# Kernel tuning notes

Measured on AMD Instinct MI355X. Metric: run time of the kernel, lower is better.

The kernel has to match this reference:

```python
import jax, jax.numpy as jnp
import numpy as np

DIM = 1024
H = 16
DH = DIM // H
LN_EPS = 1e-5


def _linear_params(key, din, dout):
    kw, kb = jax.random.split(key)
    bound = 1.0 / np.sqrt(din)
    W = jax.random.uniform(kw, (din, dout), jnp.float32, -bound, bound)
    b = jax.random.uniform(kb, (dout,), jnp.float32, -bound, bound)
    return W, b


def setup_inputs() -> dict:
    key = jax.random.key(0)
    ks = jax.random.split(key, 10)
    inp = {
        "Q": jax.random.normal(ks[0], (8, 512, DIM), jnp.float32),
        "K1": jax.random.normal(ks[1], (8, 1024, DIM), jnp.float32),
        "K2": jax.random.normal(ks[2], (8, 1024, DIM), jnp.float32),
    }
    for name, k in zip(["q", "k1", "k2", "v1", "v2", "o"], ks[3:9]):
        W, b = _linear_params(k, DIM, DIM)
        inp["W" + name] = W
        inp["b" + name] = b
    inp["g0"] = jnp.ones((DIM,), jnp.float32)
    inp["beta0"] = jnp.zeros((DIM,), jnp.float32)
    inp["g1"] = jnp.ones((DIM,), jnp.float32)
    inp["beta1"] = jnp.zeros((DIM,), jnp.float32)
    return inp


def _layernorm(x, g, b):
    m = jnp.mean(x, axis=-1, keepdims=True)
    v = jnp.mean(jnp.square(x - m), axis=-1, keepdims=True)
    return (x - m) * jax.lax.rsqrt(v + LN_EPS) * g + b


def _split_heads(x):
    # torch.cat(x.split(dh, 2), dim=0): [B,N,D] -> [H*B, N, dh], head-major on axis 0
    B, N, _ = x.shape
    return x.reshape(B, N, H, DH).transpose(2, 0, 1, 3).reshape(H * B, N, DH)


def _merge_heads(x, B):
    # inverse: torch.cat(out.split(B, 0), 2)
    _, N, _ = x.shape
    return x.reshape(H, B, N, DH).transpose(1, 2, 0, 3).reshape(B, N, DIM)


def reference(Q, K1, K2, Wq, bq, Wk1, bk1, Wk2, bk2, Wv1, bv1, Wv2, bv2, Wo, bo, g0, beta0, g1, beta1):
    B = Q.shape[0]
    Qp = Q @ Wq + bq
    # NOTE: faithful to source — V is computed from the ALREADY key-projected K_dict
    K1p = K1 @ Wk1 + bk1
    K2p = K2 @ Wk2 + bk2
    V1p = K1p @ Wv1 + bv1
    V2p = K2p @ Wv2 + bv2
    Q_ = _split_heads(Qp)                                   # [H*B, Nq, dh]
    K_ = jnp.concatenate([_split_heads(K1p), _split_heads(K2p)], axis=1)  # [H*B, Nk, dh]
    V_ = jnp.concatenate([_split_heads(V1p), _split_heads(V2p)], axis=1)
    scores = jnp.einsum("bqd,bkd->bqk", Q_, K_) / np.sqrt(DIM).astype(np.float32)
    # NOTE: faithful to source — softmax over the QUERY axis (dim=1)
    A = jax.nn.softmax(scores, axis=1)
    out = Q_ + jnp.einsum("bqk,bkd->bqd", A, V_)
    out = _merge_heads(out, B)                              # [B, Nq, DIM]
    out = _layernorm(out, g0, beta0)
    out = out + jax.nn.relu(out @ Wo + bo)
    out = _layernorm(out, g1, beta1)
    return out
```

## Files before the change

### kernel.cpp

```cpp
#include <hip/hip_runtime.h>
#include <math.h>

typedef __attribute__((ext_vector_type(8))) _Float16 half8v;
typedef __attribute__((ext_vector_type(4))) _Float16 half4v;
typedef __attribute__((ext_vector_type(4))) float f32x4;

__device__ __forceinline__ void gload16(const void* g, void* l) {
  __builtin_amdgcn_global_load_lds(
      (const __attribute__((address_space(1))) void*)g,
      (__attribute__((address_space(3))) void*)l, 16, 0, 0);
}

struct WP { const float* src; _Float16* dst; };
struct WPArgs { WP w[6]; };

__global__ __launch_bounds__(256)
void wprep_kernel(WPArgs args) {
  __shared__ float tile[32][33];
  const WP wp = args.w[blockIdx.z];
  const int t  = threadIdx.x;
  const int r  = t >> 3;
  const int c  = (t & 7) * 4;
  const int n0 = blockIdx.x * 32;
  const int k0 = blockIdx.y * 32;
  float4 v = *(const float4*)(wp.src + (size_t)(k0 + r) * 1024 + n0 + c);
  tile[r][c] = v.x; tile[r][c + 1] = v.y; tile[r][c + 2] = v.z; tile[r][c + 3] = v.w;
  __syncthreads();
  half4v h;
  #pragma unroll
  for (int i = 0; i < 4; ++i) h[i] = (_Float16)tile[c + i][r];
  *(half4v*)(wp.dst + (size_t)(n0 + r) * 1024 + k0 + c) = h;
}

__global__ __launch_bounds__(256)
void aconv_kernel(const float* __restrict__ in, _Float16* __restrict__ out, int n4) {
  int i = blockIdx.x * 256 + threadIdx.x;
  if (i >= n4) return;
  float4 v = ((const float4*)in)[i];
  half4v o;
  o[0] = (_Float16)v.x; o[1] = (_Float16)v.y; o[2] = (_Float16)v.z; o[3] = (_Float16)v.w;
  ((half4v*)out)[i] = o;
}

template<int MODE>
__global__ __launch_bounds__(256)
void gemm_fp16(const _Float16* __restrict__ A, const _Float16* __restrict__ B,
               const float* __restrict__ bias, const _Float16* __restrict__ X,
               _Float16* __restrict__ C, float* __restrict__ Cf,
               _Float16* __restrict__ Vt) {
  __shared__ _Float16 sA[8192];
  __shared__ _Float16 sB[8192];
  const int t    = threadIdx.x;
  const int bn   = blockIdx.x * 128;
  const int bm   = blockIdx.y * 128;
  const int lane = t & 63;
  const int w    = t >> 6;
  const int wr   = (w >> 1) * 64;
  const int wc   = (w & 1) * 64;
  const int lm   = lane & 15;
  const int lq   = lane >> 4;

  f32x4 acc[4][4];
  #pragma unroll
  for (int i = 0; i < 4; ++i)
    #pragma unroll
    for (int j = 0; j < 4; ++j) { f32x4 z = {0.f, 0.f, 0.f, 0.f}; acc[i][j] = z; }

  for (int k0 = 0; k0 < 1024; k0 += 64) {
    __syncthreads();
    #pragma unroll
    for (int i = 0; i < 4; ++i) {
      const int T    = w * 4 + i;
      const int kq   = T >> 1;
      const int row  = (T & 1) * 64 + lane;
      gload16(A + (size_t)(bm + row) * 1024 + k0 + kq * 8, &sA[(T * 64 + lane) * 8]);
      gload16(B + (size_t)(bn + row) * 1024 + k0 + kq * 8, &sB[(T * 64 + lane) * 8]);
    }
    __syncthreads();

    #pragma unroll
    for (int kk = 0; kk < 2; ++kk) {
      half8v af[4], bf[4];
      #pragma unroll
      for (int mi = 0; mi < 4; ++mi)
        af[mi] = *(const half8v*)&sA[((kk * 4 + lq) * 128 + wr + mi * 16 + lm) * 8];
      #pragma unroll
      for (int ni = 0; ni < 4; ++ni)
        bf[ni] = *(const half8v*)&sB[((kk * 4 + lq) * 128 + wc + ni * 16 + lm) * 8];
      #pragma unroll
      for (int mi = 0; mi < 4; ++mi)
        #pragma unroll
        for (int ni = 0; ni < 4; ++ni)
          acc[mi][ni] = __builtin_amdgcn_mfma_f32_16x16x32_f16(af[mi], bf[ni], acc[mi][ni], 0, 0, 0);
    }
  }

  float bv[4];
  #pragma unroll
  for (int ni = 0; ni < 4; ++ni) bv[ni] = bias[bn + wc + ni * 16 + lm];

  #pragma unroll
  for (int mi = 0; mi < 4; ++mi)
    #pragma unroll
    for (int ni = 0; ni < 4; ++ni) {
      const int col = bn + wc + ni * 16 + lm;
      if (MODE == 2) {
        const int row0 = bm + wr + mi * 16 + lq * 4;
        half4v pv;
        #pragma unroll
        for (int j = 0; j < 4; ++j) pv[j] = (_Float16)(acc[mi][ni][j] + bv[ni]);
        *(half4v*)(Vt + (size_t)col * 8192 + row0) = pv;
      } else {
        #pragma unroll
        for (int j = 0; j < 4; ++j) {
          const int row = bm + wr + mi * 16 + lq * 4 + j;
          const float v = acc[mi][ni][j] + bv[ni];
          const size_t idx = (size_t)row * 1024 + col;
          if (MODE == 0) C[idx] = (_Float16)v;
          else           Cf[idx] = (float)X[idx] + fmaxf(v, 0.f);
        }
      }
    }
}

__global__ __launch_bounds__(1024, 4)
void attn_mfma(const _Float16* __restrict__ Qp,
               const _Float16* __restrict__ K1p, const _Float16* __restrict__ K2p,
               const _Float16* __restrict__ VT1, const _Float16* __restrict__ VT2,
               float* __restrict__ Opart) {
  __shared__ _Float16 sK[2][2048];
  __shared__ _Float16 sV[2][2560];
  __shared__ _Float16 sP[20480];
  __shared__ float sZ[16][32];

  const int t    = threadIdx.x;
  const int lane = t & 63;
  const int w    = t >> 6;
  const int lm   = lane & 15;
  const int lq   = lane >> 4;
  const int hb   = blockIdx.x;
  const int ks   = blockIdx.y;
  const int h    = hb >> 3;
  const int b    = hb & 7;
  const int qw   = w * 32;
  const _Float16* __restrict__ K  = ks ? K2p : K1p;
  const _Float16* __restrict__ VT = ks ? VT2 : VT1;

  half8v qf[2][2];
  #pragma unroll
  for (int mi = 0; mi < 2; ++mi)
    #pragma unroll
    for (int dh = 0; dh < 2; ++dh)
      qf[mi][dh] = *(const half8v*)(Qp + (size_t)(b * 512 + qw + mi * 16 + lm) * 1024
                                       + h * 64 + dh * 32 + lq * 8);

  f32x4 o[2][4];
  #pragma unroll
  for (int i = 0; i < 2; ++i)
    #pragma unroll
    for (int j = 0; j < 4; ++j) { f32x4 z = {0.f, 0.f, 0.f, 0.f}; o[i][j] = z; }

  const int ku = t & 255;
  const int sd = ku & 31;
  const int sc = ku >> 5;
  const int vd = ku & 63;
  const int vc = (ku >> 6) & 3;
  _Float16* sPw = sP + w * 1280;

  half8v rk, rv;
  #define ISSUE_LOADS(K0)                                                                  \
    if (t < 256)      rk = *(const half8v*)(K + (size_t)(b * 1024 + (K0) + sd) * 1024 + h * 64 + sc * 8); \
    else if (t < 512) rv = *(const half8v*)(VT + (size_t)(h * 64 + vd) * 8192 + b * 1024 + (K0) + vc * 8);

  ISSUE_LOADS(0)

  for (int kt = 0; kt < 32; ++kt) {
    const int c = kt & 1;
    if (t < 256)      *(half8v*)&sK[c][(sc * 32 + sd) * 8] = rk;
    else if (t < 512) *(half8v*)&sV[c][vd * 40 + vc * 8] = rv;
    if (kt + 1 < 32) { ISSUE_LOADS((kt + 1) * 32) }
    __syncthreads();

    f32x4 s[2][2];
    #pragma unroll
    for (int i = 0; i < 2; ++i)
      #pragma unroll
      for (int j = 0; j < 2; ++j) { f32x4 z = {0.f, 0.f, 0.f, 0.f}; s[i][j] = z; }
    #pragma unroll
    for (int dh = 0; dh < 2; ++dh) {
      half8v kb[2];
      #pragma unroll
      for (int fi = 0; fi < 2; ++fi)
        kb[fi] = *(const half8v*)&sK[c][((dh * 4 + lq) * 32 + fi * 16 + lm) * 8];
      #pragma unroll
      for (int mi = 0; mi < 2; ++mi)
        #pragma unroll
        for (int fi = 0; fi < 2; ++fi)
          s[mi][fi] = __builtin_amdgcn_mfma_f32_16x16x32_f16(qf[mi][dh], kb[fi], s[mi][fi], 0, 0, 0);
    }

    float zp[2] = {0.f, 0.f};
    #pragma unroll
    for (int mi = 0; mi < 2; ++mi)
      #pragma unroll
      for (int fi = 0; fi < 2; ++fi)
        #pragma unroll
        for (int j = 0; j < 4; ++j) {
          float p = __expf(s[mi][fi][j] * 0.03125f);
          s[mi][fi][j] = p;
          zp[fi] += p;
        }
    #pragma unroll
    for (int fi = 0; fi < 2; ++fi) {
      zp[fi] += __shfl_xor(zp[fi], 16);
      zp[fi] += __shfl_xor(zp[fi], 32);
    }
    if (lane < 16) { sZ[w][lm] = zp[0]; sZ[w][16 + lm] = zp[1]; }
    __syncthreads();

    float iz = 0.f;
    if (lane < 32) {
      float z = 0.f;
      #pragma unroll
      for (int wv = 0; wv < 16; ++wv) z += sZ[wv][lane];
      iz = 1.0f / z;
    }
    const float iz0 = __shfl(iz, lm);
    const float iz1 = __shfl(iz, 16 + lm);

    #pragma unroll
    for (int mi = 0; mi < 2; ++mi)
      #pragma unroll
      for (int j = 0; j < 4; ++j) {
        const int q = mi * 16 + lq * 4 + j;
        sPw[q * 40 + lm]      = (_Float16)(s[mi][0][j] * iz0);
        sPw[q * 40 + 16 + lm] = (_Float16)(s[mi][1][j] * iz1);
      }

    half8v pa[2], vb[4];
    #pragma unroll
    for (int mi = 0; mi < 2; ++mi)
      pa[mi] = *(const half8v*)&sPw[(mi * 16 + lm) * 40 + lq * 8];
    #pragma unroll
    for (int ni = 0; ni < 4; ++ni)
      vb[ni] = *(const half8v*)&sV[c][(ni * 16 + lm) * 40 + lq * 8];
    #pragma unroll
    for (int mi = 0; mi < 2; ++mi)
      #pragma unroll
      for (int ni = 0; ni < 4; ++ni)
        o[mi][ni] = __builtin_amdgcn_mfma_f32_16x16x32_f16(pa[mi], vb[ni], o[mi][ni], 0, 0, 0);
  }
  #undef ISSUE_LOADS

  float* dst = Opart + (size_t)(ks * 128 + hb) * 512 * 64;
  #pragma unroll
  for (int mi = 0; mi < 2; ++mi)
    #pragma unroll
    for (int ni = 0; ni < 4; ++ni)
      #pragma unroll
      for (int j = 0; j < 4; ++j) {
        const int q = qw + mi * 16 + lq * 4 + j;
        const int d = ni * 16 + lm;
        dst[(size_t)q * 64 + d] = o[mi][ni][j];
      }
}

template<int MODE>
__global__ __launch_bounds__(256)
void ln_kernel(const float* __restrict__ fin, const _Float16* __restrict__ Qp,
               const float* __restrict__ g, const float* __restrict__ beta,
               _Float16* __restrict__ oh, float* __restrict__ of) {
  const int row = blockIdx.x;
  const int t = threadIdx.x;
  const int c = t * 4;
  float4 v;
  if (MODE == 0) {
    const int b  = row >> 9;
    const int n  = row & 511;
    const int hh = c >> 6;
    const int d  = c & 63;
    const int hb = hh * 8 + b;
    half4v qv = *(const half4v*)(Qp + (size_t)row * 1024 + c);
    float4 p0 = *(const float4*)&fin[((size_t)hb         * 512 + n) * 64 + d];
    float4 p1 = *(const float4*)&fin[((size_t)(128 + hb) * 512 + n) * 64 + d];
    v = make_float4((float)qv[0] + p0.x + p1.x, (float)qv[1] + p0.y + p1.y,
                    (float)qv[2] + p0.z + p1.z, (float)qv[3] + p0.w + p1.w);
  } else {
    v = *(const float4*)&fin[(size_t)row * 1024 + c];
  }
  float s  = v.x + v.y + v.z + v.w;
  float s2 = v.x * v.x + v.y * v.y + v.z * v.z + v.w * v.w;
  #pragma unroll
  for (int m = 1; m < 64; m <<= 1) { s += __shfl_xor(s, m); s2 += __shfl_xor(s2, m); }
  __shared__ float aS[4], aS2[4];
  const int wid = t >> 6;
  if ((t & 63) == 0) { aS[wid] = s; aS2[wid] = s2; }
  __syncthreads();
  s  = aS[0] + aS[1] + aS[2] + aS[3];
  s2 = aS2[0] + aS2[1] + aS2[2] + aS2[3];
  const float mean = s * (1.f / 1024.f);
  const float var  = s2 * (1.f / 1024.f) - mean * mean;
  const float rstd = rsqrtf(var + 1e-5f);
  float4 gg = *(const float4*)&g[c];
  float4 bb = *(const float4*)&beta[c];
  float4 ov = make_float4((v.x - mean) * rstd * gg.x + bb.x,
                          (v.y - mean) * rstd * gg.y + bb.y,
                          (v.z - mean) * rstd * gg.z + bb.z,
                          (v.w - mean) * rstd * gg.w + bb.w);
  const size_t oi = (size_t)row * 1024 + c;
  if (MODE == 0) {
    half4v hv;
    hv[0] = (_Float16)ov.x; hv[1] = (_Float16)ov.y;
    hv[2] = (_Float16)ov.z; hv[3] = (_Float16)ov.w;
    *(half4v*)(oh + oi) = hv;
  } else {
    *(float4*)(of + oi) = ov;
  }
}

extern "C" void kernel_launch(void* const* d_in, const int* in_sizes, int n_in,
                              void* d_out, int out_size, void* d_ws, size_t ws_size,
                              hipStream_t stream) {
  (void)in_sizes; (void)n_in; (void)out_size; (void)ws_size;
  const float* Q   = (const float*)d_in[0];
  const float* K1  = (const float*)d_in[1];
  const float* K2  = (const float*)d_in[2];
  const float* Wq  = (const float*)d_in[3];
  const float* bq  = (const float*)d_in[4];
  const float* Wk1 = (const float*)d_in[5];
  const float* bk1 = (const float*)d_in[6];
  const float* Wk2 = (const float*)d_in[7];
  const float* bk2 = (const float*)d_in[8];
  const float* Wv1 = (const float*)d_in[9];
  const float* bv1 = (const float*)d_in[10];
  const float* Wv2 = (const float*)d_in[11];
  const float* bv2 = (const float*)d_in[12];
  const float* Wo  = (const float*)d_in[13];
  const float* bo  = (const float*)d_in[14];
  const float* g0  = (const float*)d_in[15];
  const float* be0 = (const float*)d_in[16];
  const float* g1  = (const float*)d_in[17];
  const float* be1 = (const float*)d_in[18];

  char* WS = (char*)d_ws;
  const size_t MB = 1024 * 1024;
  auto S = [&](size_t off) { return (_Float16*)(WS + off); };
  _Float16 *Qc = S(0), *K1c = S(8 * MB), *K2c = S(24 * MB);
  _Float16 *Wt[6];
  for (int i = 0; i < 6; ++i) Wt[i] = S(40 * MB + i * 2 * MB);
  _Float16 *Qp  = S(52 * MB);
  _Float16 *K1p = S(60 * MB), *K2p = S(76 * MB);
  _Float16 *VT1 = S(92 * MB), *VT2 = S(108 * MB);
  float* Op = (float*)(WS + 124 * MB);
  _Float16 *x0 = S(0);
  float* tb = (float*)(WS + 8 * MB);

  WPArgs wa;
  const float* wsrc[6] = {Wq, Wk1, Wk2, Wv1, Wv2, Wo};
  for (int i = 0; i < 6; ++i) { wa.w[i].src = wsrc[i]; wa.w[i].dst = Wt[i]; }

  wprep_kernel<<<dim3(32, 32, 6), 256, 0, stream>>>(wa);
  aconv_kernel<<<dim3(4096), 256, 0, stream>>>(Q,  Qc,  1048576);
  aconv_kernel<<<dim3(8192), 256, 0, stream>>>(K1, K1c, 2097152);
  aconv_kernel<<<dim3(8192), 256, 0, stream>>>(K2, K2c, 2097152);

  gemm_fp16<0><<<dim3(8, 32), 256, 0, stream>>>(Qc,  Wt[0], bq,  nullptr, Qp,  nullptr, nullptr);
  gemm_fp16<0><<<dim3(8, 64), 256, 0, stream>>>(K1c, Wt[1], bk1, nullptr, K1p, nullptr, nullptr);
  gemm_fp16<0><<<dim3(8, 64), 256, 0, stream>>>(K2c, Wt[2], bk2, nullptr, K2p, nullptr, nullptr);
  gemm_fp16<2><<<dim3(8, 64), 256, 0, stream>>>(K1p, Wt[3], bv1, nullptr, nullptr, nullptr, VT1);
  gemm_fp16<2><<<dim3(8, 64), 256, 0, stream>>>(K2p, Wt[4], bv2, nullptr, nullptr, nullptr, VT2);

  attn_mfma<<<dim3(128, 2), dim3(1024), 0, stream>>>(Qp, K1p, K2p, VT1, VT2, Op);

  ln_kernel<0><<<dim3(4096), 256, 0, stream>>>(Op, Qp, g0, be0, x0, nullptr);
  gemm_fp16<1><<<dim3(8, 32), 256, 0, stream>>>(x0, Wt[5], bo, x0, nullptr, tb, nullptr);
  ln_kernel<1><<<dim3(4096), 256, 0, stream>>>(tb, nullptr, g1, be1, nullptr, (float*)d_out);
}
```

Before: 492.5 us.

## Swizzle GEMM blocks per XCD, stage epilogue through LDS, add MFMA priority hints

The GEMM now uses a 1D grid whose block index is remapped so that each XCD (bid&7) works on a contiguous band of M rows, which should improve L2 reuse of the A tiles. The fp16 epilogues (mode 0 and the transposed V mode 2) stage results in shared memory and then write 16-byte coalesced rows, replacing scattered 2-byte and strided 8-byte stores. The attention kernel wraps its MFMA sections in s_setprio to favour matrix issue. The LDS staging adds two barriers per block, and the remap assumes NM is divisible by 8 and exactly 8 N tiles.

```diff
diff --git a/kernel.cpp b/kernel.cpp
--- a/kernel.cpp
+++ b/kernel.cpp
@@ -47,12 +47,18 @@
 void gemm_fp16(const _Float16* __restrict__ A, const _Float16* __restrict__ B,
                const float* __restrict__ bias, const _Float16* __restrict__ X,
                _Float16* __restrict__ C, float* __restrict__ Cf,
-               _Float16* __restrict__ Vt) {
-  __shared__ _Float16 sA[8192];
-  __shared__ _Float16 sB[8192];
+               _Float16* __restrict__ Vt, int NM) {
+  __shared__ _Float16 smem[16384];
+  _Float16* const sA = smem;
+  _Float16* const sB = smem + 8192;
   const int t    = threadIdx.x;
-  const int bn   = blockIdx.x * 128;
-  const int bm   = blockIdx.y * 128;
+  const int bid  = blockIdx.x;
+  const int xcd  = bid & 7;
+  const int li   = bid >> 3;
+  const int m    = xcd * (NM >> 3) + (li >> 3);
+  const int n    = li & 7;
+  const int bm   = m * 128;
+  const int bn   = n * 128;
   const int lane = t & 63;
   const int w    = t >> 6;
   const int wr   = (w >> 1) * 64;
@@ -99,28 +105,46 @@
   #pragma unroll
   for (int ni = 0; ni < 4; ++ni) bv[ni] = bias[bn + wc + ni * 16 + lm];
 
-  #pragma unroll
-  for (int mi = 0; mi < 4; ++mi)
-    #pragma unroll
-    for (int ni = 0; ni < 4; ++ni) {
-      const int col = bn + wc + ni * 16 + lm;
-      if (MODE == 2) {
-        const int row0 = bm + wr + mi * 16 + lq * 4;
-        half4v pv;
-        #pragma unroll
-        for (int j = 0; j < 4; ++j) pv[j] = (_Float16)(acc[mi][ni][j] + bv[ni]);
-        *(half4v*)(Vt + (size_t)col * 8192 + row0) = pv;
-      } else {
+  if (MODE == 1) {
+    #pragma unroll
+    for (int mi = 0; mi < 4; ++mi)
+      #pragma unroll
+      for (int ni = 0; ni < 4; ++ni) {
+        const int col = bn + wc + ni * 16 + lm;
         #pragma unroll
         for (int j = 0; j < 4; ++j) {
           const int row = bm + wr + mi * 16 + lq * 4 + j;
-          const float v = acc[mi][ni][j] + bv[ni];
           const size_t idx = (size_t)row * 1024 + col;
-          if (MODE == 0) C[idx] = (_Float16)v;
-          else           Cf[idx] = (float)X[idx] + fmaxf(v, 0.f);
+          Cf[idx] = (float)X[idx] + fmaxf(acc[mi][ni][j] + bv[ni], 0.f);
         }
       }
-    }
+    return;
+  }
+
+  __syncthreads();
+  #pragma unroll
+  for (int mi = 0; mi < 4; ++mi)
+    #pragma unroll
+    for (int ni = 0; ni < 4; ++ni) {
+      const int cc = wc + ni * 16 + lm;
+      #pragma unroll
+      for (int j = 0; j < 4; ++j) {
+        const int rr = wr + mi * 16 + lq * 4 + j;
+        const _Float16 v = (_Float16)(acc[mi][ni][j] + bv[ni]);
+        if (MODE == 0) smem[rr * 128 + cc] = v;
+        else           smem[cc * 128 + rr] = v;
+      }
+    }
+  __syncthreads();
+  const int r16 = t >> 4;
+  const int c8  = (t & 15) * 8;
+  #pragma unroll
+  for (int p = 0; p < 8; ++p) {
+    const int row = p * 16 + r16;
+    half8v vv = *(const half8v*)&smem[row * 128 + c8];
+    if (MODE == 0) *(half8v*)(C + (size_t)(bm + row) * 1024 + bn + c8) = vv;
+    else           *(half8v*)(Vt + (size_t)(bn + row) * 8192 + bm + c8) = vv;
+  }
 }
 
 __global__ __launch_bounds__(1024, 4)
@@ -186,6 +210,7 @@
     for (int i = 0; i < 2; ++i)
       #pragma unroll
       for (int j = 0; j < 2; ++j) { f32x4 z = {0.f, 0.f, 0.f, 0.f}; s[i][j] = z; }
+    __builtin_amdgcn_s_setprio(1);
     #pragma unroll
     for (int dh = 0; dh < 2; ++dh) {
       half8v kb[2];
@@ -198,6 +223,7 @@
         for (int fi = 0; fi < 2; ++fi)
           s[mi][fi] = __builtin_amdgcn_mfma_f32_16x16x32_f16(qf[mi][dh], kb[fi], s[mi][fi], 0, 0, 0);
     }
+    __builtin_amdgcn_s_setprio(0);
 
     float zp[2] = {0.f, 0.f};
     #pragma unroll
@@ -244,11 +270,13 @@
     #pragma unroll
     for (int ni = 0; ni < 4; ++ni)
       vb[ni] = *(const half8v*)&sV[c][(ni * 16 + lm) * 40 + lq * 8];
+    __builtin_amdgcn_s_setprio(1);
     #pragma unroll
     for (int mi = 0; mi < 2; ++mi)
       #pragma unroll
       for (int ni = 0; ni < 4; ++ni)
         o[mi][ni] = __builtin_amdgcn_mfma_f32_16x16x32_f16(pa[mi], vb[ni], o[mi][ni], 0, 0, 0);
+    __builtin_amdgcn_s_setprio(0);
   }
   #undef ISSUE_LOADS
 
@@ -364,15 +392,15 @@
   aconv_kernel<<<dim3(8192), 256, 0, stream>>>(K1, K1c, 2097152);
   aconv_kernel<<<dim3(8192), 256, 0, stream>>>(K2, K2c, 2097152);
 
-  gemm_fp16<0><<<dim3(8, 32), 256, 0, stream>>>(Qc,  Wt[0], bq,  nullptr, Qp,  nullptr, nullptr);
-  gemm_fp16<0><<<dim3(8, 64), 256, 0, stream>>>(K1c, Wt[1], bk1, nullptr, K1p, nullptr, nullptr);
-  gemm_fp16<0><<<dim3(8, 64), 256, 0, stream>>>(K2c, Wt[2], bk2, nullptr, K2p, nullptr, nullptr);
-  gemm_fp16<2><<<dim3(8, 64), 256, 0, stream>>>(K1p, Wt[3], bv1, nullptr, nullptr, nullptr, VT1);
-  gemm_fp16<2><<<dim3(8, 64), 256, 0, stream>>>(K2p, Wt[4], bv2, nullptr, nullptr, nullptr, VT2);
+  gemm_fp16<0><<<dim3(256), 256, 0, stream>>>(Qc,  Wt[0], bq,  nullptr, Qp,  nullptr, nullptr, 32);
+  gemm_fp16<0><<<dim3(512), 256, 0, stream>>>(K1c, Wt[1], bk1, nullptr, K1p, nullptr, nullptr, 64);
+  gemm_fp16<0><<<dim3(512), 256, 0, stream>>>(K2c, Wt[2], bk2, nullptr, K2p, nullptr, nullptr, 64);
+  gemm_fp16<2><<<dim3(512), 256, 0, stream>>>(K1p, Wt[3], bv1, nullptr, nullptr, nullptr, VT1, 64);
+  gemm_fp16<2><<<dim3(512), 256, 0, stream>>>(K2p, Wt[4], bv2, nullptr, nullptr, nullptr, VT2, 64);
 
   attn_mfma<<<dim3(128, 2), dim3(1024), 0, stream>>>(Qp, K1p, K2p, VT1, VT2, Op);
 
   ln_kernel<0><<<dim3(4096), 256, 0, stream>>>(Op, Qp, g0, be0, x0, nullptr);
-  gemm_fp16<1><<<dim3(8, 32), 256, 0, stream>>>(x0, Wt[5], bo, x0, nullptr, tb, nullptr);
+  gemm_fp16<1><<<dim3(256), 256, 0, stream>>>(x0, Wt[5], bo, x0, nullptr, tb, nullptr, 32);
   ln_kernel<1><<<dim3(4096), 256, 0, stream>>>(tb, nullptr, g1, be1, nullptr, (float*)d_out);
 }
```

Result: no change. 488.7 us (-0.8%).
